# Optimization experiments

Hardware: AMD Instinct MI355X
Metric: run time of the kernel (lower is better)

Reference implementation:

```python
import jax, jax.numpy as jnp
from jax import lax
import numpy as np

N, C_IN, C_OUT, H, W, DS = 32, 16, 1, 128, 128, 5
NC = C_OUT * C_IN  # channels fed to DUBlock convs (= out_nc*nc_d[0])


def autocorr(x, ds):
    """x:(N,C,H,W) -> xtx_raw:(N,C,C,2ds-1,2ds-1).
    xtx_raw[n,i,j,u,v] = sum_{h,w} x[n,i,h,w] * xpad[n,j,u+h,v+w]  (zero pad ds-1),
    matching torch cal_xtx (sample-wise conv3d of x with itself)."""
    n, c, h, w = x.shape
    p = ds - 1
    xp = jnp.pad(x, ((0, 0), (0, 0), (p, p), (p, p)))
    rows = []
    for u in range(2 * ds - 1):
        cols = [jnp.einsum('nihw,njhw->nij', x,
                           lax.slice(xp, (0, 0, u, v), (n, c, u + h, v + w)))
                for v in range(2 * ds - 1)]
        rows.append(jnp.stack(cols, axis=-1))
    return jnp.stack(rows, axis=-2)  # (N,C,C,K,K), K=2ds-1


def crosscorr(x, y, ds):
    """x:(N,Ci,H,W), y:(N,Co,H,W) -> xty:(N,Co,Ci,ds,ds)  (torch cal_xty, pad=(ds-1)//2)."""
    n, c, h, w = x.shape
    p = (ds - 1) // 2
    xp = jnp.pad(x, ((0, 0), (0, 0), (p, p), (p, p)))
    rows = []
    for u in range(ds):
        cols = [jnp.einsum('nohw,njhw->noj', y,
                           lax.slice(xp, (0, 0, u, v), (n, c, u + h, v + w)))
                for v in range(ds)]
        rows.append(jnp.stack(cols, axis=-1))
    return jnp.stack(rows, axis=-2)  # (N,Co,Ci,ds,ds)


def assemble_Q(R, ds):
    """Block-Toeplitz assembly. Equivalent to torch's unfold + flip + index permutation:
    Q[n,(i,p,q),(j,oi,oj)] = R[n,i,j, ds-1+oi-p, ds-1+oj-q]."""
    n, c = R.shape[0], R.shape[1]
    r = jnp.arange(ds)
    idx = (ds - 1) + r[None, :] - r[:, None]  # idx[p,o] = ds-1+o-p in [0, 2ds-2]
    Q6 = R[:, :, :, idx[:, None, :, None], idx[None, :, None, :]]  # (N,i,j,p,q,oi,oj)
    return jnp.transpose(Q6, (0, 1, 3, 4, 2, 5, 6)).reshape(n, c * ds * ds, c * ds * ds)


def dsb(x, d, y, alpha, reg):
    """DSBlock: regularized normal equations + batched SPD solve.
    x:(N,Ci,H,W), d:(N,Co,Ci,ds,ds), y:(N,Co,H,W), alpha:(N,1,1,1), reg:(1,)"""
    n, ci, h, w = x.shape
    co, ds = d.shape[1], d.shape[-1]
    Q = assemble_Q(autocorr(x, ds), ds)                               # (N, ci*ds^2, ci*ds^2)
    P = crosscorr(x, y, ds).reshape(n, co, -1).transpose(0, 2, 1)      # (N, ci*ds^2, co)
    a = alpha.reshape(n, 1, 1) * (h * w) * reg / (ds * ds * ci)        # (N,1,1)
    m = Q.shape[1]
    Q = Q + a * jnp.eye(m, dtype=Q.dtype)
    P = P + a * d.reshape(n, co, -1).transpose(0, 2, 1)
    # torch uses cholesky + cholesky_solve on SPD Q; jnp.linalg.solve computes the
    # same solution (and its vjp matches the custom CholeskySolve backward for symmetric Q).
    D = jnp.linalg.solve(Q, P)                                         # (N, ci*ds^2, co)
    return D.reshape(n, ci, ds, ds, co).transpose(0, 4, 1, 2, 3)       # (N,Co,Ci,ds,ds)


def conv3x3(x, wgt, b):
    o = lax.conv_general_dilated(x, wgt, (1, 1), ((1, 1), (1, 1)),
                                 dimension_numbers=('NCHW', 'OIHW', 'NCHW'))
    return o + b[None, :, None, None]


def dblock_fwd(x1, x2, d, y1, y2, alpha, beta, reg,
               w1, b1, w2, b2, w3, b3, w4, b4, w5, b5, w6, b6):
    d = dsb(x1, d, y1, alpha, reg)
    d = dsb(x2, d, y2, alpha, reg)
    n, co, ci, ds = d.shape[0], d.shape[1], d.shape[2], d.shape[3]
    bmap = jnp.broadcast_to(1.0 / jnp.sqrt(beta), (n, 1, ds, ds))      # (1/beta.sqrt()).repeat
    h0 = jnp.concatenate([d.reshape(n, co * ci, ds, ds), bmap], axis=1)
    # DUBlock
    t = jax.nn.relu(conv3x3(jax.nn.relu(conv3x3(h0, w1, b1)), w2, b2))
    t = jax.nn.relu(conv3x3(jax.nn.relu(conv3x3(t, w3, b3)), w4, b4))
    t = conv3x3(jax.nn.relu(conv3x3(t, w5, b5)), w6, b6) + h0[:, :-1]
    return t.reshape(n, co, ci, ds, ds)


def setup_inputs() -> dict:
    key = jax.random.key(0)
    ks = jax.random.split(key, 24)
    inp = {
        'x1': jax.random.normal(ks[0], (N, C_IN, H, W), jnp.float32),
        'x2': jax.random.normal(ks[1], (N, C_IN, H, W), jnp.float32),
        'd': jax.random.normal(ks[2], (N, C_OUT, C_IN, DS, DS), jnp.float32),
        'y1': jax.random.normal(ks[3], (N, C_OUT, H, W), jnp.float32),
        'y2': jax.random.normal(ks[4], (N, C_OUT, H, W), jnp.float32),
        'alpha': jax.random.uniform(ks[5], (N, 1, 1, 1), jnp.float32),
        'beta': jax.random.uniform(ks[6], (N, 1, 1, 1), jnp.float32),
        'reg': jnp.ones((1,), jnp.float32),
    }
    cins = [NC + 1, NC, NC, NC, NC, NC]
    for i in range(6):
        inp['w%d' % (i + 1)] = 0.05 * jax.random.normal(ks[7 + i], (NC, cins[i], 3, 3), jnp.float32)
        inp['b%d' % (i + 1)] = jnp.zeros((NC,), jnp.float32)
    return inp


def reference(x1, x2, d, y1, y2, alpha, beta, reg,
              w1, b1, w2, b2, w3, b3, w4, b4, w5, b5, w6, b6):
    return dblock_fwd(x1, x2, d, y1, y2, alpha, beta, reg,
                      w1, b1, w2, b2, w3, b3, w4, b4, w5, b5, w6, b6)
```

## Files before the change

kernel.cpp:

```cpp
#include <hip/hip_runtime.h>
#include <hip/hip_bf16.h>

constexpr int NS   = 32;
constexpr int C    = 16;
constexpr int H    = 128;
constexpr int W    = 128;
constexpr int DS   = 5;
constexpr int M    = C * DS * DS;
constexpr int NLAG = 81;

typedef short short8 __attribute__((ext_vector_type(8)));
typedef float f32x4 __attribute__((ext_vector_type(4)));

constexpr int CH_U    = 152;
constexpr int SLOT_U  = 16 * CH_U;
constexpr int SLOT_B  = SLOT_U * 2;
constexpr int RING_B  = 16 * SLOT_B;
constexpr size_t XB_US_PER_IN = (size_t)NS * H * 16 * CH_U;

constexpr int WREP_F  = 6 * 144 * 20 + 6 * 16;
constexpr int WREP_CH = WREP_F * 4 / 16;

constexpr int PVP = 29;

__device__ __forceinline__ unsigned int pk_bf16(float a, float b) {
    union { __hip_bfloat162 h; unsigned int u; } cv;
    cv.h = __float22bfloat162_rn(make_float2(a, b));
    return cv.u;
}

__device__ __forceinline__ void gl_lds16(const void* g, void* l) {
    __builtin_amdgcn_global_load_lds(
        (const __attribute__((address_space(1))) unsigned int*)g,
        (__attribute__((address_space(3))) unsigned int*)l, 16, 0, 0);
}

__global__ __launch_bounds__(256, 1)
void prep_kernel(const float* __restrict__ x1, const float* __restrict__ x2,
                 const float* __restrict__ y1, const float* __restrict__ y2,
                 unsigned short* __restrict__ xb,
                 float* __restrict__ P1, float* __restrict__ P2,
                 const float* __restrict__ w1, const float* __restrict__ b1,
                 const float* __restrict__ w2, const float* __restrict__ b2,
                 const float* __restrict__ w3, const float* __restrict__ b3,
                 const float* __restrict__ w4, const float* __restrict__ b4,
                 const float* __restrict__ w5, const float* __restrict__ b5,
                 const float* __restrict__ w6, const float* __restrict__ b6,
                 float* __restrict__ wrep)
{
    const int b = blockIdx.x, tid = threadIdx.x;
    if (b < 1024) {
        const int n = b & 31, zi = (b >> 5) & 1, rg = b >> 6;
        const float* xn = (zi ? x2 : x1) + (size_t)n * C * H * W;
        unsigned short* dstu = xb + (size_t)zi * XB_US_PER_IN +
                               ((size_t)n * H) * SLOT_U;
        const int lrow = tid >> 5;
        const int fidx = tid & 31;
        const int grow = rg * 8 + lrow;

        float4 xv[16];
#pragma unroll
        for (int ch = 0; ch < 16; ++ch)
            xv[ch] = *(const float4*)(xn + ((size_t)ch * H + grow) * W + fidx * 4);
#pragma unroll
        for (int ch = 0; ch < 16; ++ch) {
            uint2 o;
            o.x = pk_bf16(xv[ch].x, xv[ch].y);
            o.y = pk_bf16(xv[ch].z, xv[ch].w);
            *(uint2*)(dstu + ((size_t)grow * 16 + ch) * CH_U + 8 + fidx * 4) = o;
        }
        if (tid < 128) {
            const int p = tid, prow = rg * 8 + (p >> 4), pch = p & 15;
            unsigned short* sb = dstu + ((size_t)prow * 16 + pch) * CH_U;
            *(uint4*)(sb)       = make_uint4(0u, 0u, 0u, 0u);
            *(uint4*)(sb + 136) = make_uint4(0u, 0u, 0u, 0u);
            *(uint4*)(sb + 144) = make_uint4(0u, 0u, 0u, 0u);
        }
        return;
    }
    if (b < 2048) {
        const int b2 = b - 1024;
        const int n = b2 & 31, j = (b2 >> 5) & 15, zi = b2 >> 9;
        const float* x = zi ? x2 : x1;
        const float* y = zi ? y2 : y1;
        float* P       = zi ? P2 : P1;

        const float* yn = y + (size_t)n * H * W;
        const float* xc = x + ((size_t)n * C + j) * H * W;

        const int wg = tid & 31, slab = tid >> 5;
        const int r0 = slab * 16;

        float4 yreg[20];
#pragma unroll
        for (int u = 0; u < 20; ++u) {
            const int t_ = r0 - 2 + u;
            yreg[u] = (t_ >= 0 && t_ < H)
                          ? *(const float4*)(yn + (size_t)t_ * W + wg * 4)
                          : make_float4(0.f, 0.f, 0.f, 0.f);
        }

        float acc[25];
#pragma unroll
        for (int l = 0; l < 25; ++l) acc[l] = 0.f;

#pragma unroll
        for (int rr = 0; rr < 16; ++rr) {
            const int r = r0 + rr;
            const float* xr = xc + (size_t)r * W + wg * 4;
            float w12[12];
            float4 t4 = (wg > 0) ? *(const float4*)(xr - 4) : make_float4(0, 0, 0, 0);
            w12[0] = t4.x; w12[1] = t4.y; w12[2] = t4.z; w12[3] = t4.w;
            t4 = *(const float4*)(xr);
            w12[4] = t4.x; w12[5] = t4.y; w12[6] = t4.z; w12[7] = t4.w;
            t4 = (wg < 31) ? *(const float4*)(xr + 4) : make_float4(0, 0, 0, 0);
            w12[8] = t4.x; w12[9] = t4.y; w12[10] = t4.z; w12[11] = t4.w;

#pragma unroll
            for (int u = 0; u < 5; ++u) {
                const float4 yv = yreg[rr + 4 - u];
#pragma unroll
                for (int v = 0; v < 5; ++v)
                    acc[u * 5 + v] += yv.x * w12[2 + v] + yv.y * w12[3 + v] +
                                      yv.z * w12[4 + v] + yv.w * w12[5 + v];
            }
        }

        __shared__ float red[4][25];
        const int lane = tid & 63, wv = tid >> 6;
#pragma unroll
        for (int l = 0; l < 25; ++l) {
            float v = acc[l];
#pragma unroll
            for (int off = 32; off; off >>= 1) v += __shfl_down(v, off);
            if (lane == 0) red[wv][l] = v;
        }
        __syncthreads();
        if (tid < 25)
            P[((size_t)n * C + j) * 25 + tid] = red[0][tid] + red[1][tid] + red[2][tid] + red[3][tid];
        return;
    }
    const float* wsl[6] = {w1, w2, w3, w4, w5, w6};
    const float* bsl[6] = {b1, b2, b3, b4, b5, b6};
#pragma unroll
    for (int l = 0; l < 6; ++l) {
        const int cin = (l == 0) ? 17 : 16;
        const float* ws = wsl[l];
        for (int f = tid; f < 16 * cin * 9; f += 256) {
            const int o = f / (cin * 9);
            const int rm = f - o * cin * 9;
            const int ci = rm / 9, kk = rm - ci * 9;
            wrep[l * 2880 + (o * 9 + kk) * 20 + ci] = ws[f];
        }
        if (tid < 16) wrep[17280 + l * 16 + tid] = bsl[l][tid];
    }
}

template<int P0, int P1>
__device__ __forceinline__ void autocorr_body(const unsigned short* __restrict__ xn,
                                              float* __restrict__ Rn,
                                              char* sm, int tid)
{
    constexpr int U0 = P0 / 9;
    constexpr int U1 = (P1 - 1) / 9;
    constexpr int NB = U1 - U0 + 1;
    constexpr int NP = P1 - P0;
    constexpr int SLOT_Q = SLOT_B / 16;

    unsigned short* ring = (unsigned short*)sm;
    const int lane = tid & 63;
    const int wid  = tid >> 6;
    const int q    = lane >> 4;
    const int mi   = lane & 15;
    const int rh   = wid & 3;
    const int chh  = wid >> 2;

    f32x4 acc[NP];
#pragma unroll
    for (int l = 0; l < NP; ++l) acc[l] = (f32x4){0.f, 0.f, 0.f, 0.f};

    const char* gb = (const char*)xn;

    for (int f = tid; f < 4 * SLOT_Q; f += 512)
        ((uint4*)sm)[(12 + f / SLOT_Q) * SLOT_Q + (f % SLOT_Q)] = make_uint4(0, 0, 0, 0);
    for (int f = wid; f < 38; f += 8)
        gl_lds16(gb + (size_t)f * 1024 + lane * 16, sm + f * 1024);
    __syncthreads();

    for (int s = 0; s < H; s += 4) {
        if (s < H - 8) {
            const size_t gbase = (size_t)(s + 8) * SLOT_B;
            char* lbase = sm + ((s + 8) & 15) * SLOT_B;
            for (int f = wid; f < 19; f += 8)
                gl_lds16(gb + gbase + (size_t)f * 1024 + lane * 16, lbase + f * 1024);
        } else {
            for (int f = tid; f < 4 * SLOT_Q; f += 512)
                ((uint4*)sm)[(((s + 8 + f / SLOT_Q) & 15)) * SLOT_Q + (f % SLOT_Q)] = make_uint4(0, 0, 0, 0);
        }

        const int r = s + rh;
        const unsigned short* rowA = ring + (r & 15) * SLOT_U + mi * CH_U;
#pragma unroll
        for (int cc = 0; cc < 2; ++cc) {
            const int w0 = (chh * 2 + cc) * 32;
            const uint4* pa = (const uint4*)(rowA + w0 + 8 * q);
            uint4 A0 = pa[0], A1 = pa[1], A2 = pa[2];
            unsigned int d[12] = {A0.x, A0.y, A0.z, A0.w, A1.x, A1.y, A1.z, A1.w,
                                  A2.x, A2.y, A2.z, A2.w};
            short8 bf[NB];
#pragma unroll
            for (int u = U0; u <= U1; ++u)
                bf[u - U0] = *(const short8*)(ring + ((r + u - 4 + 16) & 15) * SLOT_U +
                                              mi * CH_U + 8 + w0 + 8 * q);
#pragma unroll
            for (int v = 0; v < 9; ++v) {
                const int off = 12 - v;
                const int q4  = off >> 1;
                union { unsigned int u4[4]; short8 s8; } af;
                if (off & 1) {
#pragma unroll
                    for (int k2 = 0; k2 < 4; ++k2)
                        af.u4[k2] = (d[q4 + k2] >> 16) | (d[q4 + k2 + 1] << 16);
                } else {
#pragma unroll
                    for (int k2 = 0; k2 < 4; ++k2) af.u4[k2] = d[q4 + k2];
                }
#pragma unroll
                for (int u = U0; u <= U1; ++u) {
                    if (u * 9 + v >= P0 && u * 9 + v < P1)
                        acc[u * 9 + v - P0] = __builtin_amdgcn_mfma_f32_16x16x32_bf16(
                            af.s8, bf[u - U0], acc[u * 9 + v - P0], 0, 0, 0);
                }
            }
        }
        __syncthreads();
    }

    float* sred = (float*)sm;
#pragma unroll
    for (int cb = 0; cb < NP; cb += 9) {
        const int nc = (NP - cb < 9) ? (NP - cb) : 9;
        __syncthreads();
#pragma unroll
        for (int pp = 0; pp < 9; ++pp) {
            if (pp < nc) {
#pragma unroll
                for (int rg = 0; rg < 4; ++rg)
                    sred[(pp * 8 + wid) * 256 + (q * 4 + rg) * 16 + mi] = acc[cb + pp][rg];
            }
        }
        __syncthreads();
        if (tid < 256) {
#pragma unroll
            for (int pp = 0; pp < 9; ++pp) {
                if (pp < nc) {
                    float ssum = 0.f;
#pragma unroll
                    for (int w8 = 0; w8 < 8; ++w8)
                        ssum += sred[(pp * 8 + w8) * 256 + tid];
                    Rn[(size_t)tid * NLAG + P0 + cb + pp] = ssum;
                }
            }
        }
    }
}

__global__ __launch_bounds__(512, 2)
void autocorr_mfma(const unsigned short* __restrict__ xb,
                   float* __restrict__ R1, float* __restrict__ R2)
{
    __shared__ __align__(16) char sm[RING_B];
    const int n = blockIdx.x, zi = blockIdx.y, ug = blockIdx.z;
    const unsigned short* xn = xb + (size_t)zi * XB_US_PER_IN + (size_t)n * H * SLOT_U;
    float* Rn = (zi ? R2 : R1) + (size_t)n * C * C * NLAG;
    switch (ug) {
        case 0:  autocorr_body< 0, 20>(xn, Rn, sm, threadIdx.x); break;
        case 1:  autocorr_body<20, 40>(xn, Rn, sm, threadIdx.x); break;
        case 2:  autocorr_body<40, 60>(xn, Rn, sm, threadIdx.x); break;
        default: autocorr_body<60, 81>(xn, Rn, sm, threadIdx.x); break;
    }
}

__device__ __forceinline__ float block_sum256(float v, float* red, int t)
{
#pragma unroll
    for (int off = 32; off; off >>= 1) v += __shfl_down(v, off);
    if ((t & 63) == 0) red[t >> 6] = v;
    __syncthreads();
    float s = red[0] + red[1] + red[2] + red[3];
    __syncthreads();
    return s;
}

__device__ __forceinline__ void cg_solve(const float (&Rreg)[81],
                                         float rhs0, float rhs1,
                                         int iters, float a, int t, bool has1,
                                         float* pv, float* ap, float* red,
                                         float& z0o, float& z1o)
{
    const int jj = t & 15;
    const int e1 = t + 256;
    float z0 = 0.f, z1 = 0.f;
    float r0 = rhs0, r1 = has1 ? rhs1 : 0.f;
    float p0 = r0, p1 = r1;
    pv[(t / 25) * PVP + (t % 25)] = p0;
    if (has1) pv[(e1 / 25) * PVP + (e1 % 25)] = p1;
    float rr = block_sum256(r0 * r0 + r1 * r1, red, t);

    for (int it = 0; it < iters; ++it) {
        float pld[25], acc[25];
        const float* pj = &pv[jj * PVP];
#pragma unroll
        for (int k = 0; k < 25; ++k) pld[k] = pj[k];
#pragma unroll
        for (int k = 0; k < 25; ++k) acc[k] = 0.f;
#pragma unroll
        for (int u = 0; u < 9; ++u) {
#pragma unroll
            for (int v = 0; v < 9; ++v) {
                const float Rv = Rreg[u * 9 + v];
#pragma unroll
                for (int c = 0; c < 5; ++c) {
                    if (c < u - 4 || c > u) continue;
                    const int aa = 4 + c - u;
#pragma unroll
                    for (int dd = 0; dd < 5; ++dd) {
                        if (dd < v - 4 || dd > v) continue;
                        const int bb = 4 + dd - v;
                        acc[aa * 5 + bb] += Rv * pld[c * 5 + dd];
                    }
                }
            }
        }
#pragma unroll
        for (int k = 0; k < 25; ++k) {
            float s2 = acc[k];
            s2 += __shfl_down(s2, 8, 16);
            s2 += __shfl_down(s2, 4, 16);
            s2 += __shfl_down(s2, 2, 16);
            s2 += __shfl_down(s2, 1, 16);
            acc[k] = s2;
        }
        if (jj == 0) {
#pragma unroll
            for (int k = 0; k < 25; ++k) ap[(t >> 4) * 25 + k] = acc[k];
        }
        __syncthreads();
        const float w0 = ap[t] + a * p0;
        const float w1 = has1 ? (ap[e1] + a * p1) : 0.f;
        const float pAp = block_sum256(p0 * w0 + p1 * w1, red, t);
        const float al  = (pAp > 1e-30f) ? rr / pAp : 0.f;
        z0 += al * p0; z1 += al * p1;
        if (it + 1 < iters) {
            r0 -= al * w0; r1 -= al * w1;
            const float rrn = block_sum256(r0 * r0 + r1 * r1, red, t);
            const float be  = (rr > 1e-30f) ? rrn / rr : 0.f;
            rr = rrn;
            p0 = r0 + be * p0; p1 = r1 + be * p1;
            pv[(t / 25) * PVP + (t % 25)] = p0;
            if (has1) pv[(e1 / 25) * PVP + (e1 % 25)] = p1;
            __syncthreads();
        }
    }
    z0o = z0; z1o = z1;
}

__device__ __forceinline__ float conv_one(const float* __restrict__ act,
                                          const float* __restrict__ wall,
                                          int l, int idx)
{
    const int o = idx / 25, pix = idx % 25, yy = pix / 5, xx = pix % 5;
    float s = wall[17280 + l * 16 + o];
#pragma unroll
    for (int ky = 0; ky < 3; ++ky) {
        const int iy = yy + ky - 1;
        if ((unsigned)iy >= 5u) continue;
#pragma unroll
        for (int kx = 0; kx < 3; ++kx) {
            const int ix = xx + kx - 1;
            if ((unsigned)ix >= 5u) continue;
            const float* ip = act + (iy * 5 + ix) * 20;
            const float* wp = wall + l * 2880 + (o * 9 + ky * 3 + kx) * 20;
            const float4 a0 = *(const float4*)(ip);
            const float4 a1 = *(const float4*)(ip + 4);
            const float4 a2 = *(const float4*)(ip + 8);
            const float4 a3 = *(const float4*)(ip + 12);
            const float4 q0 = *(const float4*)(wp);
            const float4 q1 = *(const float4*)(wp + 4);
            const float4 q2 = *(const float4*)(wp + 8);
            const float4 q3 = *(const float4*)(wp + 12);
            s += a0.x * q0.x + a0.y * q0.y + a0.z * q0.z + a0.w * q0.w
               + a1.x * q1.x + a1.y * q1.y + a1.z * q1.z + a1.w * q1.w
               + a2.x * q2.x + a2.y * q2.y + a2.z * q2.z + a2.w * q2.w
               + a3.x * q3.x + a3.y * q3.y + a3.z * q3.z + a3.w * q3.w;
            if (l == 0) s += ip[16] * wp[16];
        }
    }
    return s;
}

__global__ __launch_bounds__(256, 1)
void solve_kernel(const float* __restrict__ R1, const float* __restrict__ R2,
                  const float* __restrict__ P1, const float* __restrict__ P2,
                  const float* __restrict__ d0, const float* __restrict__ alpha,
                  const float* __restrict__ beta, const float* __restrict__ reg,
                  const float* __restrict__ wrep,
                  float* __restrict__ out)
{
    __shared__ __align__(16) float Rl[256 * NLAG];
    __shared__ float pv[16 * PVP];
    __shared__ float ap[M];
    __shared__ float red[8];
    __shared__ float h0p[25 * 20];
    __shared__ float bufA[25 * 20], bufB[25 * 20];

    const int n = blockIdx.x, t = threadIdx.x;
    const bool has1 = (t < M - 256);
    const int e1 = t + 256;
    const float a = alpha[n] * (float)(H * W) * reg[0] / (float)(DS * DS * C);

    {
        const char* g = (const char*)(R1 + (size_t)n * 256 * NLAG);
        char* l = (char*)Rl;
        for (int f = t; f < 5184; f += 256)
            gl_lds16(g + (size_t)f * 16, l + (size_t)f * 16);
    }
    const float rhs10 = P1[(size_t)n * M + t] + a * d0[(size_t)n * M + t];
    const float rhs11 = has1 ? (P1[(size_t)n * M + e1] + a * d0[(size_t)n * M + e1]) : 0.f;
    __syncthreads();

    float Rreg[81];
    {
        const float* Rrow = &Rl[t * NLAG];
#pragma unroll
        for (int i = 0; i < 81; ++i) Rreg[i] = Rrow[i];
    }
    __syncthreads();

    {
        const char* g = (const char*)(R2 + (size_t)n * 256 * NLAG);
        char* l = (char*)Rl;
        for (int f = t; f < 5184; f += 256)
            gl_lds16(g + (size_t)f * 16, l + (size_t)f * 16);
    }
    float z1a, z1b;
    cg_solve(Rreg, rhs10, rhs11, 3, a, t, has1, pv, ap, red, z1a, z1b);
    {
        const float* Rrow = &Rl[t * NLAG];
#pragma unroll
        for (int i = 0; i < 81; ++i) Rreg[i] = Rrow[i];
    }
    __syncthreads();

    {
        const char* g = (const char*)wrep;
        char* l = (char*)Rl;
        for (int f = t; f < WREP_CH; f += 256)
            gl_lds16(g + (size_t)f * 16, l + (size_t)f * 16);
    }
    const float rhs20 = P2[(size_t)n * M + t] + a * z1a;
    const float rhs21 = has1 ? (P2[(size_t)n * M + e1] + a * z1b) : 0.f;
    float z20, z21;
    cg_solve(Rreg, rhs20, rhs21, 7, a, t, has1, pv, ap, red, z20, z21);

    const float* wall = (const float*)Rl;
    h0p[(t % 25) * 20 + t / 25] = z20;
    if (has1) h0p[(e1 % 25) * 20 + e1 / 25] = z21;
    if (t < 25) h0p[t * 20 + 16] = rsqrtf(beta[n]);
    __syncthreads();

#pragma unroll
    for (int l = 0; l < 6; ++l) {
        const float* act = (l == 0) ? h0p : ((l & 1) ? bufA : bufB);
        float s0 = conv_one(act, wall, l, t);
        float s1 = has1 ? conv_one(act, wall, l, e1) : 0.f;
        if (l < 5) { s0 = fmaxf(s0, 0.f); s1 = fmaxf(s1, 0.f); }
        else {
            s0 += h0p[(t % 25) * 20 + t / 25];
            if (has1) s1 += h0p[(e1 % 25) * 20 + e1 / 25];
        }
        if (l == 5) {
            out[(size_t)n * M + t] = s0;
            if (has1) out[(size_t)n * M + e1] = s1;
        } else {
            float* dstb = (l & 1) ? bufB : bufA;
            dstb[(t % 25) * 20 + t / 25] = s0;
            if (has1) dstb[(e1 % 25) * 20 + e1 / 25] = s1;
        }
        __syncthreads();
    }
}

extern "C" void kernel_launch(void* const* d_in, const int* in_sizes, int n_in,
                              void* d_out, int out_size, void* d_ws, size_t ws_size,
                              hipStream_t stream)
{
    (void)in_sizes; (void)n_in; (void)out_size; (void)ws_size;
    const float* x1    = (const float*)d_in[0];
    const float* x2    = (const float*)d_in[1];
    const float* d0    = (const float*)d_in[2];
    const float* y1    = (const float*)d_in[3];
    const float* y2    = (const float*)d_in[4];
    const float* alpha = (const float*)d_in[5];
    const float* beta  = (const float*)d_in[6];
    const float* reg   = (const float*)d_in[7];
    const float* w1 = (const float*)d_in[8];  const float* b1 = (const float*)d_in[9];
    const float* w2 = (const float*)d_in[10]; const float* b2 = (const float*)d_in[11];
    const float* w3 = (const float*)d_in[12]; const float* b3 = (const float*)d_in[13];
    const float* w4 = (const float*)d_in[14]; const float* b4 = (const float*)d_in[15];
    const float* w5 = (const float*)d_in[16]; const float* b5 = (const float*)d_in[17];
    const float* w6 = (const float*)d_in[18]; const float* b6 = (const float*)d_in[19];
    float* out = (float*)d_out;

    char* wsb = (char*)d_ws;
    unsigned short* xb = (unsigned short*)wsb;
    float* R1 = (float*)(wsb + 2 * XB_US_PER_IN * 2);
    const size_t RSZ = (size_t)NS * C * C * NLAG;
    float* R2 = R1 + RSZ;
    float* P1 = R2 + RSZ;
    float* P2 = P1 + (size_t)NS * M;
    float* wrep = P2 + (size_t)NS * M;

    prep_kernel<<<2049, 256, 0, stream>>>(x1, x2, y1, y2, xb, P1, P2,
                                          w1, b1, w2, b2, w3, b3, w4, b4,
                                          w5, b5, w6, b6, wrep);
    autocorr_mfma<<<dim3(NS, 2, 4), 512, 0, stream>>>(xb, R1, R2);
    solve_kernel<<<NS, 256, 0, stream>>>(R1, R2, P1, P2, d0, alpha, beta, reg,
                                         wrep, out);
}
```

Baseline: 273.8 us.

## Move cross-correlation blocks into autocorr kernel to overlap with MFMA work

The cross-correlation (P) computation moves out of the prep kernel and becomes extra blocks appended to the autocorrelation kernel's grid, with each block at 512 threads covering 8 rows per slab. The autocorrelation grid uses only 256 blocks on a many-CU device, so the added 1024 blocks can fill idle CUs alongside the MFMA autocorrelation work. The prep kernel also gets shorter. In exchange, the crosscorr blocks inherit the large LDS allocation and the 512-thread launch bounds, which may limit how many of them run concurrently.

```diff
diff --git a/kernel.cpp b/kernel.cpp
--- a/kernel.cpp
+++ b/kernel.cpp
@@ -37,9 +37,7 @@
 
 __global__ __launch_bounds__(256, 1)
 void prep_kernel(const float* __restrict__ x1, const float* __restrict__ x2,
-                 const float* __restrict__ y1, const float* __restrict__ y2,
                  unsigned short* __restrict__ xb,
-                 float* __restrict__ P1, float* __restrict__ P2,
                  const float* __restrict__ w1, const float* __restrict__ b1,
                  const float* __restrict__ w2, const float* __restrict__ b2,
                  const float* __restrict__ w3, const float* __restrict__ b3,
@@ -78,68 +76,6 @@
         }
         return;
     }
-    if (b < 2048) {
-        const int b2 = b - 1024;
-        const int n = b2 & 31, j = (b2 >> 5) & 15, zi = b2 >> 9;
-        const float* x = zi ? x2 : x1;
-        const float* y = zi ? y2 : y1;
-        float* P       = zi ? P2 : P1;
-
-        const float* yn = y + (size_t)n * H * W;
-        const float* xc = x + ((size_t)n * C + j) * H * W;
-
-        const int wg = tid & 31, slab = tid >> 5;
-        const int r0 = slab * 16;
-
-        float4 yreg[20];
-#pragma unroll
-        for (int u = 0; u < 20; ++u) {
-            const int t_ = r0 - 2 + u;
-            yreg[u] = (t_ >= 0 && t_ < H)
-                          ? *(const float4*)(yn + (size_t)t_ * W + wg * 4)
-                          : make_float4(0.f, 0.f, 0.f, 0.f);
-        }
-
-        float acc[25];
-#pragma unroll
-        for (int l = 0; l < 25; ++l) acc[l] = 0.f;
-
-#pragma unroll
-        for (int rr = 0; rr < 16; ++rr) {
-            const int r = r0 + rr;
-            const float* xr = xc + (size_t)r * W + wg * 4;
-            float w12[12];
-            float4 t4 = (wg > 0) ? *(const float4*)(xr - 4) : make_float4(0, 0, 0, 0);
-            w12[0] = t4.x; w12[1] = t4.y; w12[2] = t4.z; w12[3] = t4.w;
-            t4 = *(const float4*)(xr);
-            w12[4] = t4.x; w12[5] = t4.y; w12[6] = t4.z; w12[7] = t4.w;
-            t4 = (wg < 31) ? *(const float4*)(xr + 4) : make_float4(0, 0, 0, 0);
-            w12[8] = t4.x; w12[9] = t4.y; w12[10] = t4.z; w12[11] = t4.w;
-
-#pragma unroll
-            for (int u = 0; u < 5; ++u) {
-                const float4 yv = yreg[rr + 4 - u];
-#pragma unroll
-                for (int v = 0; v < 5; ++v)
-                    acc[u * 5 + v] += yv.x * w12[2 + v] + yv.y * w12[3 + v] +
-                                      yv.z * w12[4 + v] + yv.w * w12[5 + v];
-            }
-        }
-
-        __shared__ float red[4][25];
-        const int lane = tid & 63, wv = tid >> 6;
-#pragma unroll
-        for (int l = 0; l < 25; ++l) {
-            float v = acc[l];
-#pragma unroll
-            for (int off = 32; off; off >>= 1) v += __shfl_down(v, off);
-            if (lane == 0) red[wv][l] = v;
-        }
-        __syncthreads();
-        if (tid < 25)
-            P[((size_t)n * C + j) * 25 + tid] = red[0][tid] + red[1][tid] + red[2][tid] + red[3][tid];
-        return;
-    }
     const float* wsl[6] = {w1, w2, w3, w4, w5, w6};
     const float* bsl[6] = {b1, b2, b3, b4, b5, b6};
 #pragma unroll
@@ -265,19 +201,95 @@
     }
 }
 
+__device__ __forceinline__ void crosscorr_body(const float* __restrict__ yn,
+                                               const float* __restrict__ xc,
+                                               float* __restrict__ Pdst,
+                                               char* sm, int tid)
+{
+    const int wg = tid & 31, slab = tid >> 5;
+    const int r0 = slab * 8;
+
+    float4 yreg[12];
+#pragma unroll
+    for (int u = 0; u < 12; ++u) {
+        const int t_ = r0 - 2 + u;
+        yreg[u] = (t_ >= 0 && t_ < H)
+                      ? *(const float4*)(yn + (size_t)t_ * W + wg * 4)
+                      : make_float4(0.f, 0.f, 0.f, 0.f);
+    }
+
+    float acc[25];
+#pragma unroll
+    for (int l = 0; l < 25; ++l) acc[l] = 0.f;
+
+#pragma unroll
+    for (int rr = 0; rr < 8; ++rr) {
+        const int r = r0 + rr;
+        const float* xr = xc + (size_t)r * W + wg * 4;
+        float w12[12];
+        float4 t4 = (wg > 0) ? *(const float4*)(xr - 4) : make_float4(0, 0, 0, 0);
+        w12[0] = t4.x; w12[1] = t4.y; w12[2] = t4.z; w12[3] = t4.w;
+        t4 = *(const float4*)(xr);
+        w12[4] = t4.x; w12[5] = t4.y; w12[6] = t4.z; w12[7] = t4.w;
+        t4 = (wg < 31) ? *(const float4*)(xr + 4) : make_float4(0, 0, 0, 0);
+        w12[8] = t4.x; w12[9] = t4.y; w12[10] = t4.z; w12[11] = t4.w;
+
+#pragma unroll
+        for (int u = 0; u < 5; ++u) {
+            const float4 yv = yreg[rr + 4 - u];
+#pragma unroll
+            for (int v = 0; v < 5; ++v)
+                acc[u * 5 + v] += yv.x * w12[2 + v] + yv.y * w12[3 + v] +
+                                  yv.z * w12[4 + v] + yv.w * w12[5 + v];
+        }
+    }
+
+    float* red = (float*)sm;
+    const int lane = tid & 63, wv = tid >> 6;
+#pragma unroll
+    for (int l = 0; l < 25; ++l) {
+        float v = acc[l];
+#pragma unroll
+        for (int off = 32; off; off >>= 1) v += __shfl_down(v, off);
+        if (lane == 0) red[wv * 25 + l] = v;
+    }
+    __syncthreads();
+    if (tid < 25) {
+        float s = 0.f;
+#pragma unroll
+        for (int w8 = 0; w8 < 8; ++w8) s += red[w8 * 25 + tid];
+        Pdst[tid] = s;
+    }
+}
+
 __global__ __launch_bounds__(512, 2)
 void autocorr_mfma(const unsigned short* __restrict__ xb,
-                   float* __restrict__ R1, float* __restrict__ R2)
+                   const float* __restrict__ x1, const float* __restrict__ x2,
+                   const float* __restrict__ y1, const float* __restrict__ y2,
+                   float* __restrict__ R1, float* __restrict__ R2,
+                   float* __restrict__ P1, float* __restrict__ P2)
 {
     __shared__ __align__(16) char sm[RING_B];
-    const int n = blockIdx.x, zi = blockIdx.y, ug = blockIdx.z;
-    const unsigned short* xn = xb + (size_t)zi * XB_US_PER_IN + (size_t)n * H * SLOT_U;
-    float* Rn = (zi ? R2 : R1) + (size_t)n * C * C * NLAG;
-    switch (ug) {
-        case 0:  autocorr_body< 0, 20>(xn, Rn, sm, threadIdx.x); break;
-        case 1:  autocorr_body<20, 40>(xn, Rn, sm, threadIdx.x); break;
-        case 2:  autocorr_body<40, 60>(xn, Rn, sm, threadIdx.x); break;
-        default: autocorr_body<60, 81>(xn, Rn, sm, threadIdx.x); break;
+    const int b = blockIdx.x;
+    if (b < 256) {
+        const int n = b & 31, zi = (b >> 5) & 1, ug = b >> 6;
+        const unsigned short* xn = xb + (size_t)zi * XB_US_PER_IN + (size_t)n * H * SLOT_U;
+        float* Rn = (zi ? R2 : R1) + (size_t)n * C * C * NLAG;
+        switch (ug) {
+            case 0:  autocorr_body< 0, 20>(xn, Rn, sm, threadIdx.x); break;
+            case 1:  autocorr_body<20, 40>(xn, Rn, sm, threadIdx.x); break;
+            case 2:  autocorr_body<40, 60>(xn, Rn, sm, threadIdx.x); break;
+            default: autocorr_body<60, 81>(xn, Rn, sm, threadIdx.x); break;
+        }
+    } else {
+        const int c2 = b - 256;
+        const int n = c2 & 31, j = (c2 >> 5) & 15, zi = c2 >> 9;
+        const float* x = zi ? x2 : x1;
+        const float* y = zi ? y2 : y1;
+        float* P       = zi ? P2 : P1;
+        crosscorr_body(y + (size_t)n * H * W,
+                       x + ((size_t)n * C + j) * H * W,
+                       P + ((size_t)n * C + j) * 25, sm, threadIdx.x);
     }
 }
 
@@ -521,10 +533,10 @@
     float* P2 = P1 + (size_t)NS * M;
     float* wrep = P2 + (size_t)NS * M;
 
-    prep_kernel<<<2049, 256, 0, stream>>>(x1, x2, y1, y2, xb, P1, P2,
+    prep_kernel<<<1025, 256, 0, stream>>>(x1, x2, xb,
                                           w1, b1, w2, b2, w3, b3, w4, b4,
                                           w5, b5, w6, b6, wrep);
-    autocorr_mfma<<<dim3(NS, 2, 4), 512, 0, stream>>>(xb, R1, R2);
+    autocorr_mfma<<<1280, 512, 0, stream>>>(xb, x1, x2, y1, y2, R1, R2, P1, P2);
     solve_kernel<<<NS, 256, 0, stream>>>(R1, R2, P1, P2, d0, alpha, beta, reg,
                                          wrep, out);
 }
```

Result: slower. 288.4 us (+5.3%).
